# Performance work log

Hardware: AMD Instinct MI355X
Metric: run time of the kernel (lower is better)

Reference implementation:

```python
import jax, jax.numpy as jnp
import numpy as np

EPS = 1.1920929e-07  # torch.finfo(float32).eps, used by F.rms_norm default

def rope(x, cos, sin):
    # x: [B,T,H,D]; cos/sin: [1,T,1,D//2]
    d = x.shape[-1] // 2
    x1, x2 = x[..., :d], x[..., d:]
    return jnp.concatenate([x1 * cos + x2 * sin, -x1 * sin + x2 * cos], axis=-1)

def rmsnorm(x):
    return x * jax.lax.rsqrt(jnp.mean(x * x, axis=-1, keepdims=True) + EPS)

def setup_inputs() -> dict:
    key = jax.random.key(0)
    ks = jax.random.split(key, 9)
    B, T, E = 2, 2048, 1024
    Hkv, D = 4, 64
    return {
        "x": jax.random.normal(ks[0], (B, T, E), jnp.float32),
        "ve": jax.random.normal(ks[1], (B, T, Hkv * D), jnp.float32),
        "cos": jax.random.normal(ks[2], (1, T, 1, D // 2), jnp.float32),
        "sin": jax.random.normal(ks[3], (1, T, 1, D // 2), jnp.float32),
        "Wq": jax.random.normal(ks[4], (E, E), jnp.float32) * 0.02,
        "Wk": jax.random.normal(ks[5], (Hkv * D, E), jnp.float32) * 0.02,
        "Wv": jax.random.normal(ks[6], (Hkv * D, E), jnp.float32) * 0.02,
        "Wproj": jax.random.normal(ks[7], (E, E), jnp.float32) * 0.02,
        "Wgate": jax.random.normal(ks[8], (Hkv, 32), jnp.float32) * 0.02,
        "window_size": 1024,
    }

def reference(x, ve, cos, sin, Wq, Wk, Wv, Wproj, Wgate, window_size):
    B, T, E = x.shape
    H, Hkv, D = 16, 4, 64
    G = H // Hkv  # GQA group size
    q = (x @ Wq.T).reshape(B, T, H, D)
    k = (x @ Wk.T).reshape(B, T, Hkv, D)
    v = (x @ Wv.T).reshape(B, T, Hkv, D)
    # value-embedding gating
    gate = 2.0 * jax.nn.sigmoid(x[..., :32] @ Wgate.T)          # [B,T,Hkv]
    v = v + gate[..., None] * ve.reshape(B, T, Hkv, D)
    # RoPE then QK RMS-norm
    q = rmsnorm(rope(q, cos, sin))
    k = rmsnorm(rope(k, cos, sin))
    # to [B,H,T,D]; repeat-interleave kv heads for GQA (matches torch enable_gqa)
    q = q.transpose(0, 2, 1, 3)
    k = jnp.repeat(k.transpose(0, 2, 1, 3), G, axis=1)
    v = jnp.repeat(v.transpose(0, 2, 1, 3), G, axis=1)
    # causal + sliding-window boolean mask
    row = jnp.arange(T)[:, None]
    col = jnp.arange(T)[None, :]
    mask = (col <= row) & (col >= row - window_size)            # [T,T]
    scale = 1.0 / jnp.sqrt(jnp.float32(D))
    scores = jnp.einsum("bhqd,bhkd->bhqk", q, k) * scale
    scores = jnp.where(mask, scores, -jnp.inf)
    p = jax.nn.softmax(scores, axis=-1)
    y = jnp.einsum("bhqk,bhkd->bhqd", p, v)
    y = y.transpose(0, 2, 1, 3).reshape(B, T, E)
    return y @ Wproj.T
```

## Files before the change

### kernel.cpp

```cpp
#include <hip/hip_runtime.h>


typedef float f32x4 __attribute__((ext_vector_type(4)));
typedef short s16x8 __attribute__((ext_vector_type(8)));
typedef short s16x4 __attribute__((ext_vector_type(4)));
typedef _Float16 f16x4 __attribute__((ext_vector_type(4)));

__device__ __forceinline__ unsigned short f2bf(float f) {
  unsigned u = __float_as_uint(f);
  u += 0x7fffu + ((u >> 16) & 1u);
  return (unsigned short)(u >> 16);
}
__device__ __forceinline__ unsigned short h16(float f) {
  _Float16 h = (_Float16)f;
  return __builtin_bit_cast(unsigned short, h);
}

__device__ __forceinline__ float fexp2(float x) {
#if __has_builtin(__builtin_amdgcn_exp2f)
  return __builtin_amdgcn_exp2f(x);
#else
  return __expf(x * 0.69314718f);
#endif
}

__device__ __forceinline__ void gl2lds16(const unsigned short* g, unsigned short* l) {
  __builtin_amdgcn_global_load_lds((const __attribute__((address_space(1))) unsigned int*)g,
                                   (__attribute__((address_space(3))) unsigned int*)l, 16, 0, 0);
}

__global__ __launch_bounds__(256) void cvt_gate(
    const float* __restrict__ x, const float* __restrict__ wq, const float* __restrict__ wk,
    const float* __restrict__ wv, const float* __restrict__ wp, const float* __restrict__ wgate,
    unsigned short* __restrict__ xb, unsigned short* __restrict__ wqkv,
    unsigned short* __restrict__ wpj, float* __restrict__ gatep) {
  int blk = blockIdx.x;
  if (blk < 6656) {
    int i = blk * 256 + threadIdx.x;
    const float* s;
    unsigned short* d;
    if (i < 1048576) { s = x; d = xb; }
    else if (i < 1310720) { i -= 1048576; s = wq; d = wqkv; }
    else if (i < 1376256) { i -= 1310720; s = wk; d = wqkv + 1048576; }
    else if (i < 1441792) { i -= 1376256; s = wv; d = wqkv + 1310720; }
    else { i -= 1441792; s = wp; d = wpj; }
    float4 v = ((const float4*)s)[i];
    ushort4 o;
    o.x = f2bf(v.x); o.y = f2bf(v.y); o.z = f2bf(v.z); o.w = f2bf(v.w);
    ((ushort4*)d)[i] = o;
  } else {
    int i = (blk - 6656) * 256 + threadIdx.x;
    int bt = i >> 2, h = i & 3;
    const float4* xp = (const float4*)(x + (size_t)bt * 1024);
    const float4* wpt = (const float4*)(wgate + h * 32);
    float s = 0.f;
#pragma unroll
    for (int j = 0; j < 8; ++j) {
      float4 a = xp[j], b = wpt[j];
      s += a.x * b.x + a.y * b.y + a.z * b.z + a.w * b.w;
    }
    gatep[i] = 2.f / (1.f + __expf(-s));
  }
}

__global__ __launch_bounds__(256) void gemm_qkv(
    const unsigned short* __restrict__ A, const unsigned short* __restrict__ B,
    const float* __restrict__ cosp, const float* __restrict__ sinp,
    const float* __restrict__ gatep, const float* __restrict__ ve,
    unsigned short* __restrict__ q_r, unsigned short* __restrict__ k_r,
    unsigned short* __restrict__ v_r) {
  __shared__ unsigned short As[64 * 32];
  __shared__ unsigned short Bs[128 * 32];
  __shared__ unsigned short epi[4][32 * 68];
  const int K = 1024;
  int bn = blockIdx.x, bm = blockIdx.y;
  int t = threadIdx.x;
  int w = t >> 6, lane = t & 63;
  int c = lane & 15, g = lane >> 4;
  int wm = w >> 1, wn = w & 1;

  f32x4 acc[2][4];
#pragma unroll
  for (int i = 0; i < 2; ++i)
#pragma unroll
    for (int j = 0; j < 4; ++j) acc[i][j] = (f32x4){0.f, 0.f, 0.f, 0.f};

  const unsigned short* Ab = A + (size_t)(bm * 64) * K;
  const unsigned short* Bb = B + (size_t)(bn * 128) * K;
  int srow = lane >> 2;
  int scol = (lane & 3) * 8;

  for (int k0 = 0; k0 < K; k0 += 32) {
    gl2lds16(Ab + (size_t)(w * 16 + srow) * K + k0 + scol, As + w * 512);
    gl2lds16(Bb + (size_t)(w * 16 + srow) * K + k0 + scol, Bs + w * 512);
    gl2lds16(Bb + (size_t)(64 + w * 16 + srow) * K + k0 + scol, Bs + 2048 + w * 512);
    __syncthreads();
    s16x8 af[2], bf[4];
#pragma unroll
    for (int mt = 0; mt < 2; ++mt)
      af[mt] = *(const s16x8*)(As + (wm * 32 + mt * 16 + c) * 32 + g * 8);
#pragma unroll
    for (int nt = 0; nt < 4; ++nt)
      bf[nt] = *(const s16x8*)(Bs + (wn * 64 + nt * 16 + c) * 32 + g * 8);
#pragma unroll
    for (int mt = 0; mt < 2; ++mt)
#pragma unroll
      for (int nt = 0; nt < 4; ++nt)
        acc[mt][nt] = __builtin_amdgcn_mfma_f32_16x16x32_bf16(af[mt], bf[nt], acc[mt][nt], 0, 0, 0);
    __syncthreads();
  }

  const float QSCL = 0.125f * 1.44269504f;
  if (bn < 10) {
    unsigned short* eb = epi[w];
#pragma unroll
    for (int mt = 0; mt < 2; ++mt) {
#pragma unroll
      for (int r = 0; r < 4; ++r) {
        int lrow = mt * 16 + g * 4 + r;
        int rowg = bm * 64 + wm * 32 + lrow;
        int tt = rowg & 2047;
        float v0 = acc[mt][0][r], v1 = acc[mt][1][r], v2 = acc[mt][2][r], v3 = acc[mt][3][r];
        float cs0 = cosp[tt * 32 + c], sn0 = sinp[tt * 32 + c];
        float cs1 = cosp[tt * 32 + 16 + c], sn1 = sinp[tt * 32 + 16 + c];
        float r0 = v0 * cs0 + v2 * sn0;
        float r1 = v1 * cs1 + v3 * sn1;
        float r2 = v2 * cs0 - v0 * sn0;
        float r3 = v3 * cs1 - v1 * sn1;
        float ss = r0 * r0 + r1 * r1 + r2 * r2 + r3 * r3;
        ss += __shfl_xor(ss, 1);
        ss += __shfl_xor(ss, 2);
        ss += __shfl_xor(ss, 4);
        ss += __shfl_xor(ss, 8);
        float sc = rsqrtf(ss * (1.0f / 64.0f) + 1.1920929e-07f);
        if (bn < 8) sc *= QSCL;
        eb[lrow * 68 + c] = f2bf(r0 * sc);
        eb[lrow * 68 + 16 + c] = f2bf(r1 * sc);
        eb[lrow * 68 + 32 + c] = f2bf(r2 * sc);
        eb[lrow * 68 + 48 + c] = f2bf(r3 * sc);
      }
    }
    asm volatile("s_waitcnt lgkmcnt(0)" ::: "memory");
#pragma unroll
    for (int j = 0; j < 4; ++j) {
      int idx = lane * 4 + j;
      int lrow = idx >> 3;
      int ck = idx & 7;
      s16x8 val = *(const s16x8*)(eb + lrow * 68 + ck * 8);
      int rowg = bm * 64 + wm * 32 + lrow;
      int b = rowg >> 11, tt = rowg & 2047;
      unsigned short* dst;
      if (bn < 8) dst = q_r + ((size_t)(b * 16 + bn * 2 + wn) * 2048 + tt) * 64 + ck * 8;
      else dst = k_r + ((size_t)(b * 4 + (bn - 8) * 2 + wn) * 2048 + tt) * 64 + ck * 8;
      *(s16x8*)dst = val;
    }
  } else {
#pragma unroll
    for (int mt = 0; mt < 2; ++mt) {
#pragma unroll
      for (int r = 0; r < 4; ++r) {
        int rowg = bm * 64 + wm * 32 + mt * 16 + g * 4 + r;
        int b = rowg >> 11, tt = rowg & 2047;
        int h = (bn - 10) * 2 + wn;
        float gate = gatep[rowg * 4 + h];
        const float* vep = ve + (size_t)rowg * 256 + h * 64;
        unsigned short* vp = v_r + ((size_t)(b * 4 + h) * 2048 + tt) * 64;
        vp[c] = h16(acc[mt][0][r] + gate * vep[c]);
        vp[16 + c] = h16(acc[mt][1][r] + gate * vep[16 + c]);
        vp[32 + c] = h16(acc[mt][2][r] + gate * vep[32 + c]);
        vp[48 + c] = h16(acc[mt][3][r] + gate * vep[48 + c]);
      }
    }
  }
}

__global__ __launch_bounds__(256) void gemm_bf16_64(
    const unsigned short* __restrict__ A, const unsigned short* __restrict__ B,
    float* __restrict__ C, int K, int ldc) {
  __shared__ unsigned short As[64 * 32];
  __shared__ unsigned short Bs[128 * 32];
  int bn = blockIdx.x, bm = blockIdx.y;
  int t = threadIdx.x;
  int w = t >> 6, lane = t & 63;
  int c = lane & 15, g = lane >> 4;
  int wm = w >> 1, wn = w & 1;

  f32x4 acc[2][4];
#pragma unroll
  for (int i = 0; i < 2; ++i)
#pragma unroll
    for (int j = 0; j < 4; ++j) acc[i][j] = (f32x4){0.f, 0.f, 0.f, 0.f};

  const unsigned short* Ab = A + (size_t)(bm * 64) * K;
  const unsigned short* Bb = B + (size_t)(bn * 128) * K;
  int srow = lane >> 2;
  int scol = (lane & 3) * 8;

  for (int k0 = 0; k0 < K; k0 += 32) {
    gl2lds16(Ab + (size_t)(w * 16 + srow) * K + k0 + scol, As + w * 512);
    gl2lds16(Bb + (size_t)(w * 16 + srow) * K + k0 + scol, Bs + w * 512);
    gl2lds16(Bb + (size_t)(64 + w * 16 + srow) * K + k0 + scol, Bs + 2048 + w * 512);
    __syncthreads();
    s16x8 af[2], bf[4];
#pragma unroll
    for (int mt = 0; mt < 2; ++mt)
      af[mt] = *(const s16x8*)(As + (wm * 32 + mt * 16 + c) * 32 + g * 8);
#pragma unroll
    for (int nt = 0; nt < 4; ++nt)
      bf[nt] = *(const s16x8*)(Bs + (wn * 64 + nt * 16 + c) * 32 + g * 8);
#pragma unroll
    for (int mt = 0; mt < 2; ++mt)
#pragma unroll
      for (int nt = 0; nt < 4; ++nt)
        acc[mt][nt] = __builtin_amdgcn_mfma_f32_16x16x32_bf16(af[mt], bf[nt], acc[mt][nt], 0, 0, 0);
    __syncthreads();
  }
#pragma unroll
  for (int mt = 0; mt < 2; ++mt)
#pragma unroll
    for (int nt = 0; nt < 4; ++nt)
#pragma unroll
      for (int r = 0; r < 4; ++r) {
        int rowg = bm * 64 + wm * 32 + mt * 16 + g * 4 + r;
        int colg = bn * 128 + wn * 64 + nt * 16 + c;
        C[(size_t)rowg * ldc + colg] = acc[mt][nt][r];
      }
}

__global__ __launch_bounds__(256) void transpose_v(const unsigned short* __restrict__ v_r,
                                                   unsigned short* __restrict__ v_p2) {
  __shared__ unsigned short tile[64][72];
  int blk = blockIdx.x;
  int s = blk >> 5;
  int t0 = (blk & 31) * 64;
  int tt = threadIdx.x;
  int rcol = (tt & 7) * 8;
  int rrow = tt >> 3;
#pragma unroll
  for (int i = 0; i < 2; ++i) {
    int row = rrow + i * 32;
    *(s16x8*)&tile[row][rcol] = *(const s16x8*)(v_r + ((size_t)s * 2048 + t0 + row) * 64 + rcol);
  }
  __syncthreads();
#pragma unroll
  for (int i = 0; i < 2; ++i) {
    int idx = tt + i * 256;
    int ht = idx >> 8;
    int d = (idx >> 2) & 63;
    int e8 = (idx & 3) * 8;
    s16x8 o;
#pragma unroll
    for (int j = 0; j < 8; ++j) o[j] = tile[ht * 32 + e8 + j][d];
    *(s16x8*)(v_p2 + (size_t)s * 131072 + ((size_t)((t0 >> 5) + ht)) * 2048 + d * 32 + e8) = o;
  }
}

__global__ __launch_bounds__(256) void attn_kernel(
    const unsigned short* __restrict__ q_r, const unsigned short* __restrict__ k_r,
    const unsigned short* __restrict__ v_p2, unsigned short* __restrict__ y_b,
    const int* __restrict__ wptr) {
  const int W = *wptr;
  const int bid = blockIdx.x;
  const int qt = bid & 31, h = (bid >> 5) & 15, b = bid >> 9;
  const int tid = threadIdx.x;
  const int w = tid >> 6, lane = tid & 63, c = lane & 15, g = lane >> 4;
  const int r0b = qt * 64;
  const int r0w = r0b + w * 16;
  const int hkv = h >> 2;
  const float M = 11.5415603f;

  __shared__ unsigned short Ks[32 * 68];
  __shared__ unsigned short Vs[64 * 40];

  const unsigned short* kbase = k_r + (size_t)(b * 4 + hkv) * 131072;
  const unsigned short* vbase = v_p2 + (size_t)(b * 4 + hkv) * 131072;
  const unsigned short* qbase = q_r + ((size_t)(b * 16 + h) * 2048 + r0w) * 64;

  s16x8 q_lo = *(const s16x8*)(qbase + c * 64 + g * 8);
  s16x8 q_hi = *(const s16x8*)(qbase + c * 64 + 32 + g * 8);

  int kt0w = r0w - W; if (kt0w < 0) kt0w = 0;
  const int ktEw = r0w + 16;
  int KT0 = r0b - W; if (KT0 < 0) KT0 = 0;
  KT0 &= ~31;
  const int KTE = r0b + 64;

  float l_part = 0.f;
  f32x4 acc[4];
#pragma unroll
  for (int dt = 0; dt < 4; ++dt) acc[dt] = (f32x4){0.f, 0.f, 0.f, 0.f};

  s16x8 pk = *(const s16x8*)(kbase + (size_t)KT0 * 64 + tid * 8);
  s16x8 pv = *(const s16x8*)(vbase + (size_t)(KT0 >> 5) * 2048 + tid * 8);

  unsigned short* kdst = Ks + (tid >> 3) * 68 + (tid & 7) * 8;
  unsigned short* vdst = Vs + (tid >> 2) * 40 + (tid & 3) * 8;

  for (int kt = KT0; kt < KTE; kt += 32) {
    int nkt = (kt + 32 < KTE) ? kt + 32 : kt;
    s16x8 nk = *(const s16x8*)(kbase + (size_t)nkt * 64 + tid * 8);
    s16x8 nv = *(const s16x8*)(vbase + (size_t)(nkt >> 5) * 2048 + tid * 8);

    *(s16x4*)kdst = __builtin_shufflevector(pk, pk, 0, 1, 2, 3);
    *(s16x4*)(kdst + 4) = __builtin_shufflevector(pk, pk, 4, 5, 6, 7);
    *(s16x8*)vdst = pv;
    __syncthreads();

    if (kt + 32 > kt0w && kt < ktEw) {
      const unsigned short* kr0 = Ks + c * 68 + g * 8;
      s16x4 a0 = *(const s16x4*)(kr0);
      s16x4 a1 = *(const s16x4*)(kr0 + 4);
      s16x4 a2 = *(const s16x4*)(kr0 + 32);
      s16x4 a3 = *(const s16x4*)(kr0 + 36);
      const unsigned short* kr1 = kr0 + 16 * 68;
      s16x4 a4 = *(const s16x4*)(kr1);
      s16x4 a5 = *(const s16x4*)(kr1 + 4);
      s16x4 a6 = *(const s16x4*)(kr1 + 32);
      s16x4 a7 = *(const s16x4*)(kr1 + 36);
      s16x8 k0lo = __builtin_shufflevector(a0, a1, 0, 1, 2, 3, 4, 5, 6, 7);
      s16x8 k0hi = __builtin_shufflevector(a2, a3, 0, 1, 2, 3, 4, 5, 6, 7);
      s16x8 k1lo = __builtin_shufflevector(a4, a5, 0, 1, 2, 3, 4, 5, 6, 7);
      s16x8 k1hi = __builtin_shufflevector(a6, a7, 0, 1, 2, 3, 4, 5, 6, 7);

      f32x4 S0 = (f32x4){0.f, 0.f, 0.f, 0.f};
      f32x4 S1 = (f32x4){0.f, 0.f, 0.f, 0.f};
      S0 = __builtin_amdgcn_mfma_f32_16x16x32_bf16(k0lo, q_lo, S0, 0, 0, 0);
      S0 = __builtin_amdgcn_mfma_f32_16x16x32_bf16(k0hi, q_hi, S0, 0, 0, 0);
      S1 = __builtin_amdgcn_mfma_f32_16x16x32_bf16(k1lo, q_lo, S1, 0, 0, 0);
      S1 = __builtin_amdgcn_mfma_f32_16x16x32_bf16(k1hi, q_hi, S1, 0, 0, 0);

      f16x4 P0, P1;
      const bool edge = (kt < kt0w + 32) || (kt + 32 > r0w);
      const int qrow = r0w + c;
#pragma unroll
      for (int r = 0; r < 4; ++r) {
        float p0 = fexp2(S0[r] - M);
        float p1 = fexp2(S1[r] - M);
        if (edge) {
          int k0i = kt + g * 4 + r;
          int k1i = k0i + 16;
          if (!(k0i <= qrow && k0i >= qrow - W)) p0 = 0.f;
          if (!(k1i <= qrow && k1i >= qrow - W)) p1 = 0.f;
        }
        l_part += p0 + p1;
        P0[r] = (_Float16)p0;
        P1[r] = (_Float16)p1;
      }

#pragma unroll
      for (int dt = 0; dt < 4; ++dt) {
        const unsigned short* vr = Vs + (dt * 16 + c) * 40 + g * 4;
        f16x4 va = *(const f16x4*)(vr);
        f16x4 vb = *(const f16x4*)(vr + 16);
        acc[dt] = __builtin_amdgcn_mfma_f32_16x16x16f16(va, P0, acc[dt], 0, 0, 0);
        acc[dt] = __builtin_amdgcn_mfma_f32_16x16x16f16(vb, P1, acc[dt], 0, 0, 0);
      }
    }
    __syncthreads();
    pk = nk; pv = nv;
  }

  float l = l_part;
  l += __shfl_xor(l, 16);
  l += __shfl_xor(l, 32);
  float inv = 1.0f / l;

  unsigned short* ob = y_b + ((size_t)(b * 2048 + r0w + c) * 16 + h) * 64 + g * 4;
#pragma unroll
  for (int dt = 0; dt < 4; ++dt) {
    ushort4 o;
    o.x = f2bf(acc[dt][0] * inv);
    o.y = f2bf(acc[dt][1] * inv);
    o.z = f2bf(acc[dt][2] * inv);
    o.w = f2bf(acc[dt][3] * inv);
    *(ushort4*)(ob + dt * 16) = o;
  }
}

extern "C" void kernel_launch(void* const* d_in, const int* in_sizes, int n_in,
                              void* d_out, int out_size, void* d_ws, size_t ws_size,
                              hipStream_t stream) {
  const float* x = (const float*)d_in[0];
  const float* ve = (const float*)d_in[1];
  const float* cosp = (const float*)d_in[2];
  const float* sinp = (const float*)d_in[3];
  const float* Wq = (const float*)d_in[4];
  const float* Wk = (const float*)d_in[5];
  const float* Wv = (const float*)d_in[6];
  const float* Wproj = (const float*)d_in[7];
  const float* Wgate = (const float*)d_in[8];
  const int* wptr = (const int*)d_in[9];

  unsigned short* xb = (unsigned short*)d_ws;
  unsigned short* wqkv = xb + 4194304;
  unsigned short* wpj = wqkv + 1572864;
  unsigned short* q_r = wpj + 1048576;
  unsigned short* k_r = q_r + 4194304;
  unsigned short* v_r = k_r + 1048576;
  unsigned short* y_b = v_r + 1048576;
  unsigned short* vp2 = y_b + 4194304;
  float* gatep = (float*)(vp2 + 1048576);

  cvt_gate<<<6720, 256, 0, stream>>>(x, Wq, Wk, Wv, Wproj, Wgate, xb, wqkv, wpj, gatep);
  gemm_qkv<<<dim3(12, 64), 256, 0, stream>>>(xb, wqkv, cosp, sinp, gatep, ve, q_r, k_r, v_r);
  transpose_v<<<256, 256, 0, stream>>>(v_r, vp2);
  attn_kernel<<<1024, 256, 0, stream>>>(q_r, k_r, vp2, y_b, wptr);
  gemm_bf16_64<<<dim3(8, 64), 256, 0, stream>>>(y_b, wpj, (float*)d_out, 1024, 1024);
}
```

Measured before the change: 185.8 us.

## Fuse V transpose into QKV GEMM epilogue, widen K tile, double-buffer attention LDS

The QKV GEMM epilogue now writes V already transposed into the tiled layout attention expects, staging it through shared memory. This removes the separate transpose kernel and its round trip through global memory. Both GEMMs now step K by 64 with an XOR-swizzled LDS layout, which halves the number of barriers and aims to avoid bank conflicts. The attention kernel double-buffers its K/V shared tiles and drops the trailing barrier, in exchange for more LDS per block and a possible race if one barrier per iteration is not enough.

```diff
diff --git a/kernel.cpp b/kernel.cpp
--- a/kernel.cpp
+++ b/kernel.cpp
@@ -68,10 +68,10 @@
     const float* __restrict__ cosp, const float* __restrict__ sinp,
     const float* __restrict__ gatep, const float* __restrict__ ve,
     unsigned short* __restrict__ q_r, unsigned short* __restrict__ k_r,
-    unsigned short* __restrict__ v_r) {
-  __shared__ unsigned short As[64 * 32];
-  __shared__ unsigned short Bs[128 * 32];
-  __shared__ unsigned short epi[4][32 * 68];
+    unsigned short* __restrict__ vp2) {
+  __shared__ unsigned short smem[12288];
+  unsigned short* As = smem;
+  unsigned short* Bs = smem + 4096;
   const int K = 1024;
   int bn = blockIdx.x, bm = blockIdx.y;
   int t = threadIdx.x;
@@ -87,32 +87,43 @@
 
   const unsigned short* Ab = A + (size_t)(bm * 64) * K;
   const unsigned short* Bb = B + (size_t)(bn * 128) * K;
-  int srow = lane >> 2;
-  int scol = (lane & 3) * 8;
-
-  for (int k0 = 0; k0 < K; k0 += 32) {
-    gl2lds16(Ab + (size_t)(w * 16 + srow) * K + k0 + scol, As + w * 512);
-    gl2lds16(Bb + (size_t)(w * 16 + srow) * K + k0 + scol, Bs + w * 512);
-    gl2lds16(Bb + (size_t)(64 + w * 16 + srow) * K + k0 + scol, Bs + 2048 + w * 512);
+  int srow = lane >> 3;
+  int ssw = ((lane & 7) ^ srow) * 8;
+
+  for (int k0 = 0; k0 < K; k0 += 64) {
+#pragma unroll
+    for (int j = 0; j < 2; ++j) {
+      int r = w * 16 + j * 8;
+      gl2lds16(Ab + (size_t)(r + srow) * K + k0 + ssw, As + r * 64);
+    }
+#pragma unroll
+    for (int j = 0; j < 4; ++j) {
+      int r = w * 32 + j * 8;
+      gl2lds16(Bb + (size_t)(r + srow) * K + k0 + ssw, Bs + r * 64);
+    }
     __syncthreads();
-    s16x8 af[2], bf[4];
-#pragma unroll
-    for (int mt = 0; mt < 2; ++mt)
-      af[mt] = *(const s16x8*)(As + (wm * 32 + mt * 16 + c) * 32 + g * 8);
-#pragma unroll
-    for (int nt = 0; nt < 4; ++nt)
-      bf[nt] = *(const s16x8*)(Bs + (wn * 64 + nt * 16 + c) * 32 + g * 8);
-#pragma unroll
-    for (int mt = 0; mt < 2; ++mt)
+#pragma unroll
+    for (int kk = 0; kk < 2; ++kk) {
+      int sw = ((kk * 4 + g) ^ (c & 7)) * 8;
+      s16x8 af[2], bf[4];
+#pragma unroll
+      for (int mt = 0; mt < 2; ++mt)
+        af[mt] = *(const s16x8*)(As + (wm * 32 + mt * 16 + c) * 64 + sw);
 #pragma unroll
       for (int nt = 0; nt < 4; ++nt)
-        acc[mt][nt] = __builtin_amdgcn_mfma_f32_16x16x32_bf16(af[mt], bf[nt], acc[mt][nt], 0, 0, 0);
+        bf[nt] = *(const s16x8*)(Bs + (wn * 64 + nt * 16 + c) * 64 + sw);
+#pragma unroll
+      for (int mt = 0; mt < 2; ++mt)
+#pragma unroll
+        for (int nt = 0; nt < 4; ++nt)
+          acc[mt][nt] = __builtin_amdgcn_mfma_f32_16x16x32_bf16(af[mt], bf[nt], acc[mt][nt], 0, 0, 0);
+    }
     __syncthreads();
   }
 
   const float QSCL = 0.125f * 1.44269504f;
   if (bn < 10) {
-    unsigned short* eb = epi[w];
+    unsigned short* eb = smem + w * 2176;
 #pragma unroll
     for (int mt = 0; mt < 2; ++mt) {
 #pragma unroll
@@ -155,21 +166,34 @@
       *(s16x8*)dst = val;
     }
   } else {
+    unsigned short* eb = smem + w * 2560;
+    int h = (bn - 10) * 2 + wn;
 #pragma unroll
     for (int mt = 0; mt < 2; ++mt) {
 #pragma unroll
       for (int r = 0; r < 4; ++r) {
-        int rowg = bm * 64 + wm * 32 + mt * 16 + g * 4 + r;
-        int b = rowg >> 11, tt = rowg & 2047;
-        int h = (bn - 10) * 2 + wn;
+        int key = mt * 16 + g * 4 + r;
+        int rowg = bm * 64 + wm * 32 + key;
         float gate = gatep[rowg * 4 + h];
         const float* vep = ve + (size_t)rowg * 256 + h * 64;
-        unsigned short* vp = v_r + ((size_t)(b * 4 + h) * 2048 + tt) * 64;
-        vp[c] = h16(acc[mt][0][r] + gate * vep[c]);
-        vp[16 + c] = h16(acc[mt][1][r] + gate * vep[16 + c]);
-        vp[32 + c] = h16(acc[mt][2][r] + gate * vep[32 + c]);
-        vp[48 + c] = h16(acc[mt][3][r] + gate * vep[48 + c]);
+        eb[(0 * 16 + c) * 40 + key] = h16(acc[mt][0][r] + gate * vep[c]);
+        eb[(1 * 16 + c) * 40 + key] = h16(acc[mt][1][r] + gate * vep[16 + c]);
+        eb[(2 * 16 + c) * 40 + key] = h16(acc[mt][2][r] + gate * vep[32 + c]);
+        eb[(3 * 16 + c) * 40 + key] = h16(acc[mt][3][r] + gate * vep[48 + c]);
       }
+    }
+    asm volatile("s_waitcnt lgkmcnt(0)" ::: "memory");
+    int rowg0 = bm * 64 + wm * 32;
+    int b = rowg0 >> 11;
+    int tile = (rowg0 & 2047) >> 5;
+    unsigned short* vb = vp2 + ((size_t)(b * 4 + h) * 64 + tile) * 2048;
+#pragma unroll
+    for (int j = 0; j < 4; ++j) {
+      int cid = j * 64 + lane;
+      int d = cid >> 2;
+      int kg = cid & 3;
+      s16x8 val = *(const s16x8*)(eb + d * 40 + kg * 8);
+      *(s16x8*)(vb + d * 32 + kg * 8) = val;
     }
   }
 }
@@ -177,8 +201,8 @@
 __global__ __launch_bounds__(256) void gemm_bf16_64(
     const unsigned short* __restrict__ A, const unsigned short* __restrict__ B,
     float* __restrict__ C, int K, int ldc) {
-  __shared__ unsigned short As[64 * 32];
-  __shared__ unsigned short Bs[128 * 32];
+  __shared__ unsigned short As[64 * 64];
+  __shared__ unsigned short Bs[128 * 64];
   int bn = blockIdx.x, bm = blockIdx.y;
   int t = threadIdx.x;
   int w = t >> 6, lane = t & 63;
@@ -193,26 +217,37 @@
 
   const unsigned short* Ab = A + (size_t)(bm * 64) * K;
   const unsigned short* Bb = B + (size_t)(bn * 128) * K;
-  int srow = lane >> 2;
-  int scol = (lane & 3) * 8;
-
-  for (int k0 = 0; k0 < K; k0 += 32) {
-    gl2lds16(Ab + (size_t)(w * 16 + srow) * K + k0 + scol, As + w * 512);
-    gl2lds16(Bb + (size_t)(w * 16 + srow) * K + k0 + scol, Bs + w * 512);
-    gl2lds16(Bb + (size_t)(64 + w * 16 + srow) * K + k0 + scol, Bs + 2048 + w * 512);
+  int srow = lane >> 3;
+  int ssw = ((lane & 7) ^ srow) * 8;
+
+  for (int k0 = 0; k0 < K; k0 += 64) {
+#pragma unroll
+    for (int j = 0; j < 2; ++j) {
+      int r = w * 16 + j * 8;
+      gl2lds16(Ab + (size_t)(r + srow) * K + k0 + ssw, As + r * 64);
+    }
+#pragma unroll
+    for (int j = 0; j < 4; ++j) {
+      int r = w * 32 + j * 8;
+      gl2lds16(Bb + (size_t)(r + srow) * K + k0 + ssw, Bs + r * 64);
+    }
     __syncthreads();
-    s16x8 af[2], bf[4];
-#pragma unroll
-    for (int mt = 0; mt < 2; ++mt)
-      af[mt] = *(const s16x8*)(As + (wm * 32 + mt * 16 + c) * 32 + g * 8);
-#pragma unroll
-    for (int nt = 0; nt < 4; ++nt)
-      bf[nt] = *(const s16x8*)(Bs + (wn * 64 + nt * 16 + c) * 32 + g * 8);
-#pragma unroll
-    for (int mt = 0; mt < 2; ++mt)
+#pragma unroll
+    for (int kk = 0; kk < 2; ++kk) {
+      int sw = ((kk * 4 + g) ^ (c & 7)) * 8;
+      s16x8 af[2], bf[4];
+#pragma unroll
+      for (int mt = 0; mt < 2; ++mt)
+        af[mt] = *(const s16x8*)(As + (wm * 32 + mt * 16 + c) * 64 + sw);
 #pragma unroll
       for (int nt = 0; nt < 4; ++nt)
-        acc[mt][nt] = __builtin_amdgcn_mfma_f32_16x16x32_bf16(af[mt], bf[nt], acc[mt][nt], 0, 0, 0);
+        bf[nt] = *(const s16x8*)(Bs + (wn * 64 + nt * 16 + c) * 64 + sw);
+#pragma unroll
+      for (int mt = 0; mt < 2; ++mt)
+#pragma unroll
+        for (int nt = 0; nt < 4; ++nt)
+          acc[mt][nt] = __builtin_amdgcn_mfma_f32_16x16x32_bf16(af[mt], bf[nt], acc[mt][nt], 0, 0, 0);
+    }
     __syncthreads();
   }
 #pragma unroll
@@ -225,34 +260,6 @@
         int colg = bn * 128 + wn * 64 + nt * 16 + c;
         C[(size_t)rowg * ldc + colg] = acc[mt][nt][r];
       }
-}
-
-__global__ __launch_bounds__(256) void transpose_v(const unsigned short* __restrict__ v_r,
-                                                   unsigned short* __restrict__ v_p2) {
-  __shared__ unsigned short tile[64][72];
-  int blk = blockIdx.x;
-  int s = blk >> 5;
-  int t0 = (blk & 31) * 64;
-  int tt = threadIdx.x;
-  int rcol = (tt & 7) * 8;
-  int rrow = tt >> 3;
-#pragma unroll
-  for (int i = 0; i < 2; ++i) {
-    int row = rrow + i * 32;
-    *(s16x8*)&tile[row][rcol] = *(const s16x8*)(v_r + ((size_t)s * 2048 + t0 + row) * 64 + rcol);
-  }
-  __syncthreads();
-#pragma unroll
-  for (int i = 0; i < 2; ++i) {
-    int idx = tt + i * 256;
-    int ht = idx >> 8;
-    int d = (idx >> 2) & 63;
-    int e8 = (idx & 3) * 8;
-    s16x8 o;
-#pragma unroll
-    for (int j = 0; j < 8; ++j) o[j] = tile[ht * 32 + e8 + j][d];
-    *(s16x8*)(v_p2 + (size_t)s * 131072 + ((size_t)((t0 >> 5) + ht)) * 2048 + d * 32 + e8) = o;
-  }
 }
 
 __global__ __launch_bounds__(256) void attn_kernel(
@@ -269,8 +276,8 @@
   const int hkv = h >> 2;
   const float M = 11.5415603f;
 
-  __shared__ unsigned short Ks[32 * 68];
-  __shared__ unsigned short Vs[64 * 40];
+  __shared__ unsigned short Ks[2][32 * 68];
+  __shared__ unsigned short Vs[2][64 * 40];
 
   const unsigned short* kbase = k_r + (size_t)(b * 4 + hkv) * 131072;
   const unsigned short* vbase = v_p2 + (size_t)(b * 4 + hkv) * 131072;
@@ -293,21 +300,23 @@
   s16x8 pk = *(const s16x8*)(kbase + (size_t)KT0 * 64 + tid * 8);
   s16x8 pv = *(const s16x8*)(vbase + (size_t)(KT0 >> 5) * 2048 + tid * 8);
 
-  unsigned short* kdst = Ks + (tid >> 3) * 68 + (tid & 7) * 8;
-  unsigned short* vdst = Vs + (tid >> 2) * 40 + (tid & 3) * 8;
-
-  for (int kt = KT0; kt < KTE; kt += 32) {
+  const int koff = (tid >> 3) * 68 + (tid & 7) * 8;
+  const int voff = (tid >> 2) * 40 + (tid & 3) * 8;
+
+  int bufI = 0;
+  for (int kt = KT0; kt < KTE; kt += 32, bufI ^= 1) {
     int nkt = (kt + 32 < KTE) ? kt + 32 : kt;
     s16x8 nk = *(const s16x8*)(kbase + (size_t)nkt * 64 + tid * 8);
     s16x8 nv = *(const s16x8*)(vbase + (size_t)(nkt >> 5) * 2048 + tid * 8);
 
+    unsigned short* kdst = &Ks[bufI][koff];
     *(s16x4*)kdst = __builtin_shufflevector(pk, pk, 0, 1, 2, 3);
     *(s16x4*)(kdst + 4) = __builtin_shufflevector(pk, pk, 4, 5, 6, 7);
-    *(s16x8*)vdst = pv;
+    *(s16x8*)(&Vs[bufI][voff]) = pv;
     __syncthreads();
 
     if (kt + 32 > kt0w && kt < ktEw) {
-      const unsigned short* kr0 = Ks + c * 68 + g * 8;
+      const unsigned short* kr0 = &Ks[bufI][c * 68 + g * 8];
       s16x4 a0 = *(const s16x4*)(kr0);
       s16x4 a1 = *(const s16x4*)(kr0 + 4);
       s16x4 a2 = *(const s16x4*)(kr0 + 32);
@@ -349,14 +358,13 @@
 
 #pragma unroll
       for (int dt = 0; dt < 4; ++dt) {
-        const unsigned short* vr = Vs + (dt * 16 + c) * 40 + g * 4;
+        const unsigned short* vr = &Vs[bufI][(dt * 16 + c) * 40 + g * 4];
         f16x4 va = *(const f16x4*)(vr);
         f16x4 vb = *(const f16x4*)(vr + 16);
         acc[dt] = __builtin_amdgcn_mfma_f32_16x16x16f16(va, P0, acc[dt], 0, 0, 0);
         acc[dt] = __builtin_amdgcn_mfma_f32_16x16x16f16(vb, P1, acc[dt], 0, 0, 0);
       }
     }
-    __syncthreads();
     pk = nk; pv = nv;
   }
 
@@ -396,14 +404,12 @@
   unsigned short* wpj = wqkv + 1572864;
   unsigned short* q_r = wpj + 1048576;
   unsigned short* k_r = q_r + 4194304;
-  unsigned short* v_r = k_r + 1048576;
-  unsigned short* y_b = v_r + 1048576;
+  unsigned short* y_b = k_r + 1048576;
   unsigned short* vp2 = y_b + 4194304;
   float* gatep = (float*)(vp2 + 1048576);
 
   cvt_gate<<<6720, 256, 0, stream>>>(x, Wq, Wk, Wv, Wproj, Wgate, xb, wqkv, wpj, gatep);
-  gemm_qkv<<<dim3(12, 64), 256, 0, stream>>>(xb, wqkv, cosp, sinp, gatep, ve, q_r, k_r, v_r);
-  transpose_v<<<256, 256, 0, stream>>>(v_r, vp2);
+  gemm_qkv<<<dim3(12, 64), 256, 0, stream>>>(xb, wqkv, cosp, sinp, gatep, ve, q_r, k_r, vp2);
   attn_kernel<<<1024, 256, 0, stream>>>(q_r, k_r, vp2, y_b, wptr);
   gemm_bf16_64<<<dim3(8, 64), 256, 0, stream>>>(y_b, wpj, (float*)d_out, 1024, 1024);
 }
```

Measured after the change: 173.0 us. -6.9%, faster.
